# Kernel optimization log

Hardware: AMD Instinct MI355X
Metric: run time of the kernel (lower is better)

## Reference

```python
import jax, jax.numpy as jnp
import numpy as np

B, S, V, D, H, L = 256, 512, 32000, 100, 75, 128

def setup_inputs() -> dict:
    key = jax.random.key(0)
    ks = jax.random.split(key, 10)
    def lin(k, out_f, in_f):
        bound = 1.0 / np.sqrt(in_f)
        kw, kb = jax.random.split(k)
        W = jax.random.uniform(kw, (out_f, in_f), jnp.float32, -bound, bound)
        b = jax.random.uniform(kb, (out_f,), jnp.float32, -bound, bound)
        return W, b
    W1, b1 = lin(ks[0], H, D)   # i2h_fc1
    W2, b2 = lin(ks[1], H, H)   # i2h_fc2
    Wo, bo = lin(ks[2], H, H)   # h2o_fc
    Wfc, bfc = lin(ks[3], L, H) # fc
    emb = jax.random.normal(ks[4], (V, D), jnp.float32)
    X = jax.random.randint(ks[5], (B, S), 0, V)
    return {"X": X, "emb": emb, "W1": W1, "b1": b1, "W2": W2, "b2": b2,
            "Wo": Wo, "bo": bo, "Wfc": Wfc, "bfc": bfc}

def reference(X, emb, W1, b1, W2, b2, Wo, bo, Wfc, bfc):
    x = emb[X]                                   # [B,S,D] embedding lookup (dropout off: is_training=False)
    xp = jnp.einsum('bsd,hd->bsh', x, W1) + b1   # precompute input projection for all steps
    h0 = jnp.zeros((X.shape[0], W2.shape[0]), x.dtype)

    def step(h, xp_t):
        h = jax.nn.sigmoid(xp_t + h @ W2.T + b2)       # Elman hidden update
        o = jax.nn.sigmoid(h @ Wo.T + bo)              # per-step output
        return h, o

    _, outs = jax.lax.scan(step, h0, jnp.swapaxes(xp, 0, 1))  # [S,B,H]
    outs = jnp.swapaxes(outs, 0, 1)                            # [B,S,H] (batch_first)
    return jnp.einsum('bsh,lh->bsl', outs, Wfc) + bfc          # [B,S,L]
```

## Files before the change

### kernel.cpp

```cpp
#include <hip/hip_runtime.h>
#include <hip/hip_bf16.h>

typedef unsigned int uint;
typedef unsigned short ushort;

constexpr int Bn = 256, Sn = 512, Vn = 32000, Dn = 100, Hn = 75, Ln = 128;
constexpr int EW = 80;
constexpr int KP = 96;
constexpr int W2S = 80;

constexpr size_t OFF_EMBW = 0;
constexpr size_t OFF_HALL = OFF_EMBW + (size_t)Vn*EW;
constexpr size_t OFF_W2P  = OFF_HALL + (size_t)Bn*Sn*KP/2;
constexpr size_t OFF_WOH  = OFF_W2P + 3200;
constexpr size_t OFF_WFH  = OFF_WOH + 3840;

typedef __attribute__((ext_vector_type(2))) _Float16 half2_t;
typedef __attribute__((ext_vector_type(8))) _Float16 half8;
typedef __attribute__((ext_vector_type(4))) float floatx4;

__device__ __forceinline__ ushort f2h(float f){
    union { _Float16 h; ushort u; } v; v.h = (_Float16)f; return v.u;
}
__device__ __forceinline__ half8 as_h8(uint4 u){
    union { uint4 u; half8 h; } v; v.u = u; return v.h;
}
__device__ __forceinline__ float sigmoidf(float z){
    return __builtin_amdgcn_rcpf(1.f + __expf(-z));
}

__global__ __launch_bounds__(256) void k_wprep(
    const float* __restrict__ W2, const float* __restrict__ Wo,
    const float* __restrict__ Wfc, ushort* __restrict__ w2p,
    ushort* __restrict__ woh, ushort* __restrict__ wfh, ushort* __restrict__ h_all)
{
    const int tid = blockIdx.x*256 + threadIdx.x;
    const int stride = gridDim.x*256;
    for (int i = tid; i < 80*W2S; i += stride){
        int r = i / W2S, k = i % W2S;
        w2p[i] = (r < Hn && k < Hn) ? f2h(W2[r*Hn + k]) : (ushort)0;
    }
    for (int i = tid; i < 80*KP; i += stride){
        int r = i / KP, k = i % KP;
        woh[i] = (r < Hn && k < Hn) ? f2h(Wo[r*Hn + k]) : (ushort)0;
    }
    for (int i = tid; i < Ln*KP; i += stride){
        int l = i / KP, k = i % KP;
        wfh[i] = (k < Hn) ? f2h(Wfc[l*Hn + k]) : (ushort)0;
    }
    uint* hu = (uint*)h_all;
    for (int i = tid; i < Bn*Sn*8; i += stride){
        int row = i >> 3, c = i & 7;
        hu[(size_t)row*48 + 40 + c] = 0u;
    }
}

__global__ __attribute__((amdgpu_flat_work_group_size(64,64)))
__attribute__((amdgpu_waves_per_eu(1,1)))
void k_embproj(
    const float* __restrict__ emb, const float* __restrict__ W1,
    const float* __restrict__ b1, const float* __restrict__ b2,
    float* __restrict__ embW)
{
    const int lane = threadIdx.x;
    const int v = blockIdx.x*64 + lane;
    const float4* ev = (const float4*)(emb + (size_t)v*Dn);
    float e[Dn];
    #pragma unroll
    for (int q = 0; q < Dn/4; ++q){
        float4 x = ev[q];
        e[4*q] = x.x; e[4*q+1] = x.y; e[4*q+2] = x.z; e[4*q+3] = x.w;
    }
    __shared__ float s_out[64*EW];
    #pragma unroll 4
    for (int j = 0; j < Hn; ++j){
        float a0 = b1[j] + b2[j], a1 = 0.f, a2 = 0.f, a3 = 0.f;
        const float* w = W1 + j*Dn;
        #pragma unroll
        for (int d = 0; d < Dn; d += 4){
            a0 += w[d]*e[d];     a1 += w[d+1]*e[d+1];
            a2 += w[d+2]*e[d+2]; a3 += w[d+3]*e[d+3];
        }
        s_out[lane*EW + j] = (a0+a1) + (a2+a3);
    }
    #pragma unroll
    for (int j = Hn; j < EW; ++j) s_out[lane*EW + j] = 0.f;
    __syncthreads();
    float* dst = embW + (size_t)blockIdx.x*64*EW;
    for (int i = lane; i < 64*EW; i += 64) dst[i] = s_out[i];
}

__global__ __attribute__((amdgpu_flat_work_group_size(64,64)))
__attribute__((amdgpu_waves_per_eu(1,1)))
void k_rnn(
    const int* __restrict__ X, const float* __restrict__ embW,
    const ushort* __restrict__ w2p, ushort* __restrict__ h_all)
{
    const int b = blockIdx.x;
    const int L = threadIdx.x;
    const int m = L & 15;
    const int g = L >> 4;
    __shared__ int sX[Sn];
    __shared__ __align__(16) float xpb[2][64*80];

    for (int i = L; i < Sn; i += 64) sX[i] = X[b*Sn + i];

    half8 bfr[5][3];
    #pragma unroll
    for (int t = 0; t < 5; ++t){
        #pragma unroll
        for (int ks = 0; ks < 3; ++ks){
            int k0 = ks*32 + g*8;
            half8 bv = {};
            if (k0 < 80) bv = *(const half8*)(w2p + (size_t)(16*t + m)*W2S + k0);
            bfr[t][ks] = bv;
        }
    }
    __syncthreads();

    auto stage = [&](int c){
        float* buf = xpb[c & 1];
        const int base = c*64;
        #pragma unroll
        for (int k = 0; k < 20; ++k){
            int idx = k*64 + L;
            int cs  = idx / 20;
            int off = idx - cs*20;
            int tok = sX[base + cs];
            const float* src = embW + (size_t)tok*EW + off*4;
            __builtin_amdgcn_global_load_lds(
                (const __attribute__((address_space(1))) uint*)src,
                (__attribute__((address_space(3))) uint*)(buf + k*256),
                16, 0, 0);
        }
    };

    int va0 = 32*g,      va1 = 32*g + 8,  va2 = 32*g + 16, va3 = 32*g + 24;
    int vb0 = va0 + 128, vb1 = va1 + 128, vb2 = va2 + 128, vb3 = va3 + 128;

    ushort* hout = h_all + (size_t)b*Sn*KP;
    const floatx4 zero4 = {};
    uint4 A0 = {}, A1 = {}, A2 = {};

    stage(0);
    for (int c = 0; c < 8; ++c){
        __syncthreads();
        if (c < 7) stage(c + 1);
        const float* xp = xpb[c & 1];
        float x1c = xp[L];
        float x2c = (L < 16) ? xp[64 + L] : 0.f;
        float x1n = xp[80 + L];
        float x2n = (L < 16) ? xp[80 + 64 + L] : 0.f;
        for (int t = 0; t < 64; ++t){
            int pf = (t + 2 < 64) ? t + 2 : 63;
            float x1f = xp[pf*80 + L];
            float x2f = (L < 16) ? xp[pf*80 + 64 + L] : 0.f;

            half8 af0 = as_h8(A0), af1 = as_h8(A1), af2 = as_h8(A2);

            floatx4 acc0, acc1, acc2, acc3, acc4;
            acc0 = __builtin_amdgcn_mfma_f32_16x16x32_f16(af0, bfr[0][0], zero4, 0,0,0);
            acc1 = __builtin_amdgcn_mfma_f32_16x16x32_f16(af0, bfr[1][0], zero4, 0,0,0);
            acc2 = __builtin_amdgcn_mfma_f32_16x16x32_f16(af0, bfr[2][0], zero4, 0,0,0);
            acc3 = __builtin_amdgcn_mfma_f32_16x16x32_f16(af0, bfr[3][0], zero4, 0,0,0);
            acc4 = __builtin_amdgcn_mfma_f32_16x16x32_f16(af0, bfr[4][0], zero4, 0,0,0);
            acc0 = __builtin_amdgcn_mfma_f32_16x16x32_f16(af1, bfr[0][1], acc0, 0,0,0);
            acc1 = __builtin_amdgcn_mfma_f32_16x16x32_f16(af1, bfr[1][1], acc1, 0,0,0);
            acc2 = __builtin_amdgcn_mfma_f32_16x16x32_f16(af1, bfr[2][1], acc2, 0,0,0);
            acc3 = __builtin_amdgcn_mfma_f32_16x16x32_f16(af1, bfr[3][1], acc3, 0,0,0);
            acc4 = __builtin_amdgcn_mfma_f32_16x16x32_f16(af1, bfr[4][1], acc4, 0,0,0);
            acc0 = __builtin_amdgcn_mfma_f32_16x16x32_f16(af2, bfr[0][2], acc0, 0,0,0);
            acc1 = __builtin_amdgcn_mfma_f32_16x16x32_f16(af2, bfr[1][2], acc1, 0,0,0);
            acc2 = __builtin_amdgcn_mfma_f32_16x16x32_f16(af2, bfr[2][2], acc2, 0,0,0);
            acc3 = __builtin_amdgcn_mfma_f32_16x16x32_f16(af2, bfr[3][2], acc3, 0,0,0);
            acc4 = __builtin_amdgcn_mfma_f32_16x16x32_f16(af2, bfr[4][2], acc4, 0,0,0);

            float y1 = (L < 32) ? ((L < 16) ? acc0[0] : acc1[0])
                                : ((L < 48) ? acc2[0] : acc3[0]);
            float y2 = acc4[0];

            float h1 = sigmoidf(y1 + x1c);
            float h2 = sigmoidf(y2 + x2c);
            if (L >= 11) h2 = 0.f;
            ushort u1 = f2h(h1);
            ushort u2 = f2h(h2);
            int s = c*64 + t;
            hout[(size_t)s*KP + L] = u1;
            if (L < 16) hout[(size_t)s*KP + 64 + L] = u2;

            uint v1 = u1, v2 = u2;
            uint pr1 = (uint)__builtin_amdgcn_update_dpp(0, (int)v1, 0xB1, 0xF, 0xF, true);
            uint pr2 = (uint)__builtin_amdgcn_update_dpp(0, (int)v2, 0xB1, 0xF, 0xF, true);
            int q1 = (int)(v1 | (pr1 << 16));
            int q2 = (int)(v2 | (pr2 << 16));

            A0.x = (uint)__builtin_amdgcn_ds_bpermute(va0, q1);
            A0.y = (uint)__builtin_amdgcn_ds_bpermute(va1, q1);
            A0.z = (uint)__builtin_amdgcn_ds_bpermute(va2, q1);
            A0.w = (uint)__builtin_amdgcn_ds_bpermute(va3, q1);
            A1.x = (uint)__builtin_amdgcn_ds_bpermute(vb0, q1);
            A1.y = (uint)__builtin_amdgcn_ds_bpermute(vb1, q1);
            A1.z = (uint)__builtin_amdgcn_ds_bpermute(vb2, q1);
            A1.w = (uint)__builtin_amdgcn_ds_bpermute(vb3, q1);
            A2.x = (uint)__builtin_amdgcn_ds_bpermute(va0, q2);
            A2.y = (uint)__builtin_amdgcn_ds_bpermute(va1, q2);
            A2.z = (uint)__builtin_amdgcn_ds_bpermute(va2, q2);
            A2.w = (uint)__builtin_amdgcn_ds_bpermute(va3, q2);

            x1c = x1n; x2c = x2n; x1n = x1f; x2n = x2f;
        }
    }
}

__global__ __launch_bounds__(256) void k_out(
    const ushort* __restrict__ h_all, const ushort* __restrict__ woh,
    const ushort* __restrict__ wfh, const float* __restrict__ bo,
    const float* __restrict__ bfc, float* __restrict__ out)
{
    const int lane = threadIdx.x & 63;
    const int w    = threadIdx.x >> 6;
    const size_t r0 = (size_t)blockIdx.x*64 + w*16;
    const int m = lane & 15;
    const int g = lane >> 4;
    __shared__ __align__(16) ushort o_lds[4][16*104];
    ushort* ot = o_lds[w];
    for (int i = lane; i < 128; i += 64){
        int row = i >> 3, cw = i & 7;
        *(uint*)&ot[row*104 + 80 + cw*2] = 0u;
    }
    floatx4 acc1[5] = {};
    const ushort* hbase = h_all + r0*KP;
    #pragma unroll
    for (int ks = 0; ks < 3; ++ks){
        half8 a = *(const half8*)(hbase + (size_t)m*KP + ks*32 + g*8);
        #pragma unroll
        for (int t = 0; t < 5; ++t){
            half8 bt = *(const half8*)(woh + (16*t + m)*KP + ks*32 + g*8);
            acc1[t] = __builtin_amdgcn_mfma_f32_16x16x32_f16(a, bt, acc1[t], 0, 0, 0);
        }
    }
    #pragma unroll
    for (int t = 0; t < 5; ++t){
        int n = 16*t + m;
        float bias = (n < Hn) ? bo[n] : 0.f;
        #pragma unroll
        for (int r = 0; r < 4; ++r){
            int row = g*4 + r;
            float o = 1.f/(1.f + __expf(-(acc1[t][r] + bias)));
            if (n >= Hn) o = 0.f;
            ot[row*104 + n] = f2h(o);
        }
    }
    floatx4 acc2[8] = {};
    #pragma unroll
    for (int ks = 0; ks < 3; ++ks){
        half8 a = *(const half8*)(ot + m*104 + ks*32 + g*8);
        #pragma unroll
        for (int t = 0; t < 8; ++t){
            half8 bt = *(const half8*)(wfh + (16*t + m)*KP + ks*32 + g*8);
            acc2[t] = __builtin_amdgcn_mfma_f32_16x16x32_f16(a, bt, acc2[t], 0, 0, 0);
        }
    }
    float* orow = out + r0*Ln;
    #pragma unroll
    for (int t = 0; t < 8; ++t){
        float bias = bfc[16*t + m];
        #pragma unroll
        for (int r = 0; r < 4; ++r){
            int row = g*4 + r;
            orow[(size_t)row*Ln + 16*t + m] = acc2[t][r] + bias;
        }
    }
}

extern "C" void kernel_launch(void* const* d_in, const int* in_sizes, int n_in,
                              void* d_out, int out_size, void* d_ws, size_t ws_size,
                              hipStream_t stream)
{
    const int*   X   = (const int*)d_in[0];
    const float* emb = (const float*)d_in[1];
    const float* W1  = (const float*)d_in[2];
    const float* b1  = (const float*)d_in[3];
    const float* W2  = (const float*)d_in[4];
    const float* b2  = (const float*)d_in[5];
    const float* Wo  = (const float*)d_in[6];
    const float* bo  = (const float*)d_in[7];
    const float* Wfc = (const float*)d_in[8];
    const float* bfc = (const float*)d_in[9];
    float* out = (float*)d_out;
    float* ws  = (float*)d_ws;

    float*  embW = ws + OFF_EMBW;
    ushort* hall = (ushort*)(ws + OFF_HALL);
    ushort* w2p  = (ushort*)(ws + OFF_W2P);
    ushort* woh  = (ushort*)(ws + OFF_WOH);
    ushort* wfh  = (ushort*)(ws + OFF_WFH);

    k_wprep<<<dim3(512), dim3(256), 0, stream>>>(W2, Wo, Wfc, w2p, woh, wfh, hall);
    k_embproj<<<dim3(Vn/64), dim3(64), 0, stream>>>(emb, W1, b1, b2, embW);
    k_rnn<<<dim3(Bn), dim3(64), 0, stream>>>(X, embW, w2p, hall);
    k_out<<<dim3((Bn*Sn)/64), dim3(256), 0, stream>>>(hall, woh, wfh, bo, bfc, out);
}
```

Measured before the change: 352.8 us.

## Shorten RNN recurrence critical path and split embedding projection across four waves

The recurrent step now computes all five 16-wide hidden chunks in every lane group, with the input projection folded into the MFMA accumulator init. The three K-slices are summed afterwards instead of being chained through the accumulator, which removes the serial MFMA dependency. Hidden-state redistribution now uses v_permlane32_swap plus a single set of bpermute offsets instead of two offset sets. Separately, the embedding projection kernel uses 256 threads, with each wave computing about a quarter of the hidden outputs, to add parallelism per block. The cost is more sigmoid and conversion work per lane, more MFMAs with zero accumulators, and inline asm that depends on gfx950's permlane32 swap.

```diff
diff --git a/kernel.cpp b/kernel.cpp
--- a/kernel.cpp
+++ b/kernel.cpp
@@ -55,14 +55,15 @@
     }
 }
 
-__global__ __attribute__((amdgpu_flat_work_group_size(64,64)))
+__global__ __attribute__((amdgpu_flat_work_group_size(256,256)))
 __attribute__((amdgpu_waves_per_eu(1,1)))
 void k_embproj(
     const float* __restrict__ emb, const float* __restrict__ W1,
     const float* __restrict__ b1, const float* __restrict__ b2,
     float* __restrict__ embW)
 {
-    const int lane = threadIdx.x;
+    const int lane = threadIdx.x & 63;
+    const int w    = threadIdx.x >> 6;
     const int v = blockIdx.x*64 + lane;
     const float4* ev = (const float4*)(emb + (size_t)v*Dn);
     float e[Dn];
@@ -72,22 +73,27 @@
         e[4*q] = x.x; e[4*q+1] = x.y; e[4*q+2] = x.z; e[4*q+3] = x.w;
     }
     __shared__ float s_out[64*EW];
-    #pragma unroll 4
-    for (int j = 0; j < Hn; ++j){
+    const int j0 = w*19;
+    const int jend = (w == 3) ? 18 : 19;
+    #pragma unroll 2
+    for (int jj = 0; jj < jend; ++jj){
+        int j = j0 + jj;
         float a0 = b1[j] + b2[j], a1 = 0.f, a2 = 0.f, a3 = 0.f;
-        const float* w = W1 + j*Dn;
+        const float* wp = W1 + j*Dn;
         #pragma unroll
         for (int d = 0; d < Dn; d += 4){
-            a0 += w[d]*e[d];     a1 += w[d+1]*e[d+1];
-            a2 += w[d+2]*e[d+2]; a3 += w[d+3]*e[d+3];
+            a0 += wp[d]*e[d];     a1 += wp[d+1]*e[d+1];
+            a2 += wp[d+2]*e[d+2]; a3 += wp[d+3]*e[d+3];
         }
         s_out[lane*EW + j] = (a0+a1) + (a2+a3);
     }
-    #pragma unroll
-    for (int j = Hn; j < EW; ++j) s_out[lane*EW + j] = 0.f;
+    if (w == 3){
+        #pragma unroll
+        for (int j = Hn; j < EW; ++j) s_out[lane*EW + j] = 0.f;
+    }
     __syncthreads();
     float* dst = embW + (size_t)blockIdx.x*64*EW;
-    for (int i = lane; i < 64*EW; i += 64) dst[i] = s_out[i];
+    for (int i = threadIdx.x; i < 64*EW; i += 256) dst[i] = s_out[i];
 }
 
 __global__ __attribute__((amdgpu_flat_work_group_size(64,64)))
@@ -135,11 +141,11 @@
         }
     };
 
-    int va0 = 32*g,      va1 = 32*g + 8,  va2 = 32*g + 16, va3 = 32*g + 24;
-    int vb0 = va0 + 128, vb1 = va1 + 128, vb2 = va2 + 128, vb3 = va3 + 128;
+    const int vbase = (L & 32) + ((L & 16) >> 1);
+    const int va0 = 4*(vbase + 0), va1 = 4*(vbase + 2),
+              va2 = 4*(vbase + 4), va3 = 4*(vbase + 6);
 
     ushort* hout = h_all + (size_t)b*Sn*KP;
-    const floatx4 zero4 = {};
     uint4 A0 = {}, A1 = {}, A2 = {};
 
     stage(0);
@@ -147,67 +153,86 @@
         __syncthreads();
         if (c < 7) stage(c + 1);
         const float* xp = xpb[c & 1];
-        float x1c = xp[L];
-        float x2c = (L < 16) ? xp[64 + L] : 0.f;
-        float x1n = xp[80 + L];
-        float x2n = (L < 16) ? xp[80 + 64 + L] : 0.f;
+        float xc0 = xp[m], xc1 = xp[16+m], xc2 = xp[32+m], xc3 = xp[48+m], xc4 = xp[64+m];
+        float xn0 = xp[80+m], xn1 = xp[96+m], xn2 = xp[112+m], xn3 = xp[128+m], xn4 = xp[144+m];
         for (int t = 0; t < 64; ++t){
             int pf = (t + 2 < 64) ? t + 2 : 63;
-            float x1f = xp[pf*80 + L];
-            float x2f = (L < 16) ? xp[pf*80 + 64 + L] : 0.f;
+            const float* xpf = xp + pf*80;
+            float xf0 = xpf[m],    xf1 = xpf[16+m], xf2 = xpf[32+m],
+                  xf3 = xpf[48+m], xf4 = xpf[64+m];
 
             half8 af0 = as_h8(A0), af1 = as_h8(A1), af2 = as_h8(A2);
 
-            floatx4 acc0, acc1, acc2, acc3, acc4;
-            acc0 = __builtin_amdgcn_mfma_f32_16x16x32_f16(af0, bfr[0][0], zero4, 0,0,0);
-            acc1 = __builtin_amdgcn_mfma_f32_16x16x32_f16(af0, bfr[1][0], zero4, 0,0,0);
-            acc2 = __builtin_amdgcn_mfma_f32_16x16x32_f16(af0, bfr[2][0], zero4, 0,0,0);
-            acc3 = __builtin_amdgcn_mfma_f32_16x16x32_f16(af0, bfr[3][0], zero4, 0,0,0);
-            acc4 = __builtin_amdgcn_mfma_f32_16x16x32_f16(af0, bfr[4][0], zero4, 0,0,0);
-            acc0 = __builtin_amdgcn_mfma_f32_16x16x32_f16(af1, bfr[0][1], acc0, 0,0,0);
-            acc1 = __builtin_amdgcn_mfma_f32_16x16x32_f16(af1, bfr[1][1], acc1, 0,0,0);
-            acc2 = __builtin_amdgcn_mfma_f32_16x16x32_f16(af1, bfr[2][1], acc2, 0,0,0);
-            acc3 = __builtin_amdgcn_mfma_f32_16x16x32_f16(af1, bfr[3][1], acc3, 0,0,0);
-            acc4 = __builtin_amdgcn_mfma_f32_16x16x32_f16(af1, bfr[4][1], acc4, 0,0,0);
-            acc0 = __builtin_amdgcn_mfma_f32_16x16x32_f16(af2, bfr[0][2], acc0, 0,0,0);
-            acc1 = __builtin_amdgcn_mfma_f32_16x16x32_f16(af2, bfr[1][2], acc1, 0,0,0);
-            acc2 = __builtin_amdgcn_mfma_f32_16x16x32_f16(af2, bfr[2][2], acc2, 0,0,0);
-            acc3 = __builtin_amdgcn_mfma_f32_16x16x32_f16(af2, bfr[3][2], acc3, 0,0,0);
-            acc4 = __builtin_amdgcn_mfma_f32_16x16x32_f16(af2, bfr[4][2], acc4, 0,0,0);
-
-            float y1 = (L < 32) ? ((L < 16) ? acc0[0] : acc1[0])
-                                : ((L < 48) ? acc2[0] : acc3[0]);
-            float y2 = acc4[0];
-
-            float h1 = sigmoidf(y1 + x1c);
-            float h2 = sigmoidf(y2 + x2c);
-            if (L >= 11) h2 = 0.f;
-            ushort u1 = f2h(h1);
-            ushort u2 = f2h(h2);
+            floatx4 ci0 = {xc0,xc0,xc0,xc0}, ci1 = {xc1,xc1,xc1,xc1},
+                    ci2 = {xc2,xc2,xc2,xc2}, ci3 = {xc3,xc3,xc3,xc3},
+                    ci4 = {xc4,xc4,xc4,xc4};
+            const floatx4 z4 = {};
+            floatx4 p00 = __builtin_amdgcn_mfma_f32_16x16x32_f16(af0, bfr[0][0], ci0, 0,0,0);
+            floatx4 p10 = __builtin_amdgcn_mfma_f32_16x16x32_f16(af0, bfr[1][0], ci1, 0,0,0);
+            floatx4 p20 = __builtin_amdgcn_mfma_f32_16x16x32_f16(af0, bfr[2][0], ci2, 0,0,0);
+            floatx4 p30 = __builtin_amdgcn_mfma_f32_16x16x32_f16(af0, bfr[3][0], ci3, 0,0,0);
+            floatx4 p40 = __builtin_amdgcn_mfma_f32_16x16x32_f16(af0, bfr[4][0], ci4, 0,0,0);
+            floatx4 p01 = __builtin_amdgcn_mfma_f32_16x16x32_f16(af1, bfr[0][1], z4, 0,0,0);
+            floatx4 p11 = __builtin_amdgcn_mfma_f32_16x16x32_f16(af1, bfr[1][1], z4, 0,0,0);
+            floatx4 p21 = __builtin_amdgcn_mfma_f32_16x16x32_f16(af1, bfr[2][1], z4, 0,0,0);
+            floatx4 p31 = __builtin_amdgcn_mfma_f32_16x16x32_f16(af1, bfr[3][1], z4, 0,0,0);
+            floatx4 p41 = __builtin_amdgcn_mfma_f32_16x16x32_f16(af1, bfr[4][1], z4, 0,0,0);
+            floatx4 p02 = __builtin_amdgcn_mfma_f32_16x16x32_f16(af2, bfr[0][2], z4, 0,0,0);
+            floatx4 p12 = __builtin_amdgcn_mfma_f32_16x16x32_f16(af2, bfr[1][2], z4, 0,0,0);
+            floatx4 p22 = __builtin_amdgcn_mfma_f32_16x16x32_f16(af2, bfr[2][2], z4, 0,0,0);
+            floatx4 p32 = __builtin_amdgcn_mfma_f32_16x16x32_f16(af2, bfr[3][2], z4, 0,0,0);
+            floatx4 p42 = __builtin_amdgcn_mfma_f32_16x16x32_f16(af2, bfr[4][2], z4, 0,0,0);
+
+            float h0 = sigmoidf((p00[0] + p01[0]) + p02[0]);
+            float h1 = sigmoidf((p10[0] + p11[0]) + p12[0]);
+            float h2 = sigmoidf((p20[0] + p21[0]) + p22[0]);
+            float h3 = sigmoidf((p30[0] + p31[0]) + p32[0]);
+            float h4 = sigmoidf((p40[0] + p41[0]) + p42[0]);
+            if (m >= 11) h4 = 0.f;
+
+            ushort u0 = f2h(h0), u1 = f2h(h1), u2 = f2h(h2),
+                   u3 = f2h(h3), u4 = f2h(h4);
+
+            ushort us = (L < 32) ? ((L < 16) ? u0 : u1)
+                                 : ((L < 48) ? u2 : u3);
             int s = c*64 + t;
-            hout[(size_t)s*KP + L] = u1;
-            if (L < 16) hout[(size_t)s*KP + 64 + L] = u2;
-
-            uint v1 = u1, v2 = u2;
-            uint pr1 = (uint)__builtin_amdgcn_update_dpp(0, (int)v1, 0xB1, 0xF, 0xF, true);
-            uint pr2 = (uint)__builtin_amdgcn_update_dpp(0, (int)v2, 0xB1, 0xF, 0xF, true);
-            int q1 = (int)(v1 | (pr1 << 16));
-            int q2 = (int)(v2 | (pr2 << 16));
-
-            A0.x = (uint)__builtin_amdgcn_ds_bpermute(va0, q1);
-            A0.y = (uint)__builtin_amdgcn_ds_bpermute(va1, q1);
-            A0.z = (uint)__builtin_amdgcn_ds_bpermute(va2, q1);
-            A0.w = (uint)__builtin_amdgcn_ds_bpermute(va3, q1);
-            A1.x = (uint)__builtin_amdgcn_ds_bpermute(vb0, q1);
-            A1.y = (uint)__builtin_amdgcn_ds_bpermute(vb1, q1);
-            A1.z = (uint)__builtin_amdgcn_ds_bpermute(vb2, q1);
-            A1.w = (uint)__builtin_amdgcn_ds_bpermute(vb3, q1);
-            A2.x = (uint)__builtin_amdgcn_ds_bpermute(va0, q2);
-            A2.y = (uint)__builtin_amdgcn_ds_bpermute(va1, q2);
-            A2.z = (uint)__builtin_amdgcn_ds_bpermute(va2, q2);
-            A2.w = (uint)__builtin_amdgcn_ds_bpermute(va3, q2);
-
-            x1c = x1n; x2c = x2n; x1n = x1f; x2n = x2f;
+            hout[(size_t)s*KP + L] = us;
+            if (L < 16) hout[(size_t)s*KP + 64 + L] = u4;
+
+            uint pq0, pq1, pq2, pq3, pq4;
+            {
+                uint w0=u0, w1=u1, w2=u2, w3=u3, w4=u4;
+                uint r0 = (uint)__builtin_amdgcn_update_dpp(0, (int)w0, 0xB1, 0xF, 0xF, true);
+                uint r1 = (uint)__builtin_amdgcn_update_dpp(0, (int)w1, 0xB1, 0xF, 0xF, true);
+                uint r2 = (uint)__builtin_amdgcn_update_dpp(0, (int)w2, 0xB1, 0xF, 0xF, true);
+                uint r3 = (uint)__builtin_amdgcn_update_dpp(0, (int)w3, 0xB1, 0xF, 0xF, true);
+                uint r4 = (uint)__builtin_amdgcn_update_dpp(0, (int)w4, 0xB1, 0xF, 0xF, true);
+                pq0 = w0 | (r0 << 16); pq1 = w1 | (r1 << 16);
+                pq2 = w2 | (r2 << 16); pq3 = w3 | (r3 << 16);
+                pq4 = w4 | (r4 << 16);
+            }
+            uint S = pq0, Sb = pq1, T = pq2, Tb = pq3, U = pq4, Ub = 0u;
+            asm volatile("s_nop 1\n\t"
+                         "v_permlane32_swap_b32 %0, %1\n\t"
+                         "v_permlane32_swap_b32 %2, %3\n\t"
+                         "v_permlane32_swap_b32 %4, %5"
+                         : "+v"(S), "+v"(Sb), "+v"(T), "+v"(Tb), "+v"(U), "+v"(Ub));
+
+            A0.x = (uint)__builtin_amdgcn_ds_bpermute(va0, (int)S);
+            A0.y = (uint)__builtin_amdgcn_ds_bpermute(va1, (int)S);
+            A0.z = (uint)__builtin_amdgcn_ds_bpermute(va2, (int)S);
+            A0.w = (uint)__builtin_amdgcn_ds_bpermute(va3, (int)S);
+            A1.x = (uint)__builtin_amdgcn_ds_bpermute(va0, (int)T);
+            A1.y = (uint)__builtin_amdgcn_ds_bpermute(va1, (int)T);
+            A1.z = (uint)__builtin_amdgcn_ds_bpermute(va2, (int)T);
+            A1.w = (uint)__builtin_amdgcn_ds_bpermute(va3, (int)T);
+            A2.x = (uint)__builtin_amdgcn_ds_bpermute(va0, (int)U);
+            A2.y = (uint)__builtin_amdgcn_ds_bpermute(va1, (int)U);
+            A2.z = (uint)__builtin_amdgcn_ds_bpermute(va2, (int)U);
+            A2.w = (uint)__builtin_amdgcn_ds_bpermute(va3, (int)U);
+
+            xc0=xn0; xc1=xn1; xc2=xn2; xc3=xn3; xc4=xn4;
+            xn0=xf0; xn1=xf1; xn2=xf2; xn3=xf3; xn4=xf4;
         }
     }
 }
@@ -297,7 +322,7 @@
     ushort* wfh  = (ushort*)(ws + OFF_WFH);
 
     k_wprep<<<dim3(512), dim3(256), 0, stream>>>(W2, Wo, Wfc, w2p, woh, wfh, hall);
-    k_embproj<<<dim3(Vn/64), dim3(64), 0, stream>>>(emb, W1, b1, b2, embW);
+    k_embproj<<<dim3(Vn/64), dim3(256), 0, stream>>>(emb, W1, b1, b2, embW);
     k_rnn<<<dim3(Bn), dim3(64), 0, stream>>>(X, embW, w2p, hall);
     k_out<<<dim3((Bn*Sn)/64), dim3(256), 0, stream>>>(hall, woh, wfh, bo, bfc, out);
 }
```

After: 395.8 us. 1.12x slower.

## Fuse output projection into RNN kernel and widen embedding projection blocks

Applied to the files above, without the earlier changes.

The output-head kernel is folded into the tail of the recurrent kernel. Each block now has four waves: wave 0 runs the sequential recurrence, all four waves share the embedding staging, and after the loop all four compute the output head for their batch row. The embedding projection kernel is also split across four waves by hidden unit. This removes one launch and spreads projection work across more waves. The cost is that three waves sit idle during the recurrence, and the output head, previously spread over many blocks, now runs on only 256 blocks after the serial part ends.

```diff
diff --git a/kernel.cpp b/kernel.cpp
--- a/kernel.cpp
+++ b/kernel.cpp
@@ -55,14 +55,15 @@
     }
 }
 
-__global__ __attribute__((amdgpu_flat_work_group_size(64,64)))
+__global__ __attribute__((amdgpu_flat_work_group_size(256,256)))
 __attribute__((amdgpu_waves_per_eu(1,1)))
 void k_embproj(
     const float* __restrict__ emb, const float* __restrict__ W1,
     const float* __restrict__ b1, const float* __restrict__ b2,
     float* __restrict__ embW)
 {
-    const int lane = threadIdx.x;
+    const int lane = threadIdx.x & 63;
+    const int w    = threadIdx.x >> 6;
     const int v = blockIdx.x*64 + lane;
     const float4* ev = (const float4*)(emb + (size_t)v*Dn);
     float e[Dn];
@@ -72,48 +73,61 @@
         e[4*q] = x.x; e[4*q+1] = x.y; e[4*q+2] = x.z; e[4*q+3] = x.w;
     }
     __shared__ float s_out[64*EW];
-    #pragma unroll 4
-    for (int j = 0; j < Hn; ++j){
+    const int j0 = w*19;
+    const int jend = (w == 3) ? 18 : 19;
+    #pragma unroll 2
+    for (int jj = 0; jj < jend; ++jj){
+        int j = j0 + jj;
         float a0 = b1[j] + b2[j], a1 = 0.f, a2 = 0.f, a3 = 0.f;
-        const float* w = W1 + j*Dn;
+        const float* wp = W1 + j*Dn;
         #pragma unroll
         for (int d = 0; d < Dn; d += 4){
-            a0 += w[d]*e[d];     a1 += w[d+1]*e[d+1];
-            a2 += w[d+2]*e[d+2]; a3 += w[d+3]*e[d+3];
+            a0 += wp[d]*e[d];     a1 += wp[d+1]*e[d+1];
+            a2 += wp[d+2]*e[d+2]; a3 += wp[d+3]*e[d+3];
         }
         s_out[lane*EW + j] = (a0+a1) + (a2+a3);
     }
-    #pragma unroll
-    for (int j = Hn; j < EW; ++j) s_out[lane*EW + j] = 0.f;
+    if (w == 3){
+        #pragma unroll
+        for (int j = Hn; j < EW; ++j) s_out[lane*EW + j] = 0.f;
+    }
     __syncthreads();
     float* dst = embW + (size_t)blockIdx.x*64*EW;
-    for (int i = lane; i < 64*EW; i += 64) dst[i] = s_out[i];
-}
-
-__global__ __attribute__((amdgpu_flat_work_group_size(64,64)))
+    for (int i = threadIdx.x; i < 64*EW; i += 256) dst[i] = s_out[i];
+}
+
+__global__ __attribute__((amdgpu_flat_work_group_size(256,256)))
 __attribute__((amdgpu_waves_per_eu(1,1)))
 void k_rnn(
     const int* __restrict__ X, const float* __restrict__ embW,
-    const ushort* __restrict__ w2p, ushort* __restrict__ h_all)
+    const ushort* __restrict__ w2p, ushort* __restrict__ h_all,
+    const ushort* __restrict__ woh, const ushort* __restrict__ wfh,
+    const float* __restrict__ bo, const float* __restrict__ bfc,
+    float* __restrict__ out)
 {
-    const int b = blockIdx.x;
-    const int L = threadIdx.x;
-    const int m = L & 15;
-    const int g = L >> 4;
+    const int b   = blockIdx.x;
+    const int tid = threadIdx.x;
+    const int L   = tid & 63;
+    const int wv  = tid >> 6;
+    const int m   = L & 15;
+    const int g   = L >> 4;
     __shared__ int sX[Sn];
     __shared__ __align__(16) float xpb[2][64*80];
-
-    for (int i = L; i < Sn; i += 64) sX[i] = X[b*Sn + i];
+    __shared__ __align__(16) ushort o_lds[4][16*104];
+
+    for (int i = tid; i < Sn; i += 256) sX[i] = X[b*Sn + i];
 
     half8 bfr[5][3];
-    #pragma unroll
-    for (int t = 0; t < 5; ++t){
-        #pragma unroll
-        for (int ks = 0; ks < 3; ++ks){
-            int k0 = ks*32 + g*8;
-            half8 bv = {};
-            if (k0 < 80) bv = *(const half8*)(w2p + (size_t)(16*t + m)*W2S + k0);
-            bfr[t][ks] = bv;
+    if (wv == 0){
+        #pragma unroll
+        for (int t = 0; t < 5; ++t){
+            #pragma unroll
+            for (int ks = 0; ks < 3; ++ks){
+                int k0 = ks*32 + g*8;
+                half8 bv = {};
+                if (k0 < 80) bv = *(const half8*)(w2p + (size_t)(16*t + m)*W2S + k0);
+                bfr[t][ks] = bv;
+            }
         }
     }
     __syncthreads();
@@ -122,15 +136,15 @@
         float* buf = xpb[c & 1];
         const int base = c*64;
         #pragma unroll
-        for (int k = 0; k < 20; ++k){
-            int idx = k*64 + L;
+        for (int k = 0; k < 5; ++k){
+            int idx = k*256 + tid;
             int cs  = idx / 20;
             int off = idx - cs*20;
             int tok = sX[base + cs];
             const float* src = embW + (size_t)tok*EW + off*4;
             __builtin_amdgcn_global_load_lds(
                 (const __attribute__((address_space(1))) uint*)src,
-                (__attribute__((address_space(3))) uint*)(buf + k*256),
+                (__attribute__((address_space(3))) uint*)(buf + idx*4),
                 16, 0, 0);
         }
     };
@@ -146,129 +160,123 @@
     for (int c = 0; c < 8; ++c){
         __syncthreads();
         if (c < 7) stage(c + 1);
-        const float* xp = xpb[c & 1];
-        float x1c = xp[L];
-        float x2c = (L < 16) ? xp[64 + L] : 0.f;
-        float x1n = xp[80 + L];
-        float x2n = (L < 16) ? xp[80 + 64 + L] : 0.f;
-        for (int t = 0; t < 64; ++t){
-            int pf = (t + 2 < 64) ? t + 2 : 63;
-            float x1f = xp[pf*80 + L];
-            float x2f = (L < 16) ? xp[pf*80 + 64 + L] : 0.f;
-
-            half8 af0 = as_h8(A0), af1 = as_h8(A1), af2 = as_h8(A2);
-
-            floatx4 acc0, acc1, acc2, acc3, acc4;
-            acc0 = __builtin_amdgcn_mfma_f32_16x16x32_f16(af0, bfr[0][0], zero4, 0,0,0);
-            acc1 = __builtin_amdgcn_mfma_f32_16x16x32_f16(af0, bfr[1][0], zero4, 0,0,0);
-            acc2 = __builtin_amdgcn_mfma_f32_16x16x32_f16(af0, bfr[2][0], zero4, 0,0,0);
-            acc3 = __builtin_amdgcn_mfma_f32_16x16x32_f16(af0, bfr[3][0], zero4, 0,0,0);
-            acc4 = __builtin_amdgcn_mfma_f32_16x16x32_f16(af0, bfr[4][0], zero4, 0,0,0);
-            acc0 = __builtin_amdgcn_mfma_f32_16x16x32_f16(af1, bfr[0][1], acc0, 0,0,0);
-            acc1 = __builtin_amdgcn_mfma_f32_16x16x32_f16(af1, bfr[1][1], acc1, 0,0,0);
-            acc2 = __builtin_amdgcn_mfma_f32_16x16x32_f16(af1, bfr[2][1], acc2, 0,0,0);
-            acc3 = __builtin_amdgcn_mfma_f32_16x16x32_f16(af1, bfr[3][1], acc3, 0,0,0);
-            acc4 = __builtin_amdgcn_mfma_f32_16x16x32_f16(af1, bfr[4][1], acc4, 0,0,0);
-            acc0 = __builtin_amdgcn_mfma_f32_16x16x32_f16(af2, bfr[0][2], acc0, 0,0,0);
-            acc1 = __builtin_amdgcn_mfma_f32_16x16x32_f16(af2, bfr[1][2], acc1, 0,0,0);
-            acc2 = __builtin_amdgcn_mfma_f32_16x16x32_f16(af2, bfr[2][2], acc2, 0,0,0);
-            acc3 = __builtin_amdgcn_mfma_f32_16x16x32_f16(af2, bfr[3][2], acc3, 0,0,0);
-            acc4 = __builtin_amdgcn_mfma_f32_16x16x32_f16(af2, bfr[4][2], acc4, 0,0,0);
-
-            float y1 = (L < 32) ? ((L < 16) ? acc0[0] : acc1[0])
-                                : ((L < 48) ? acc2[0] : acc3[0]);
-            float y2 = acc4[0];
-
-            float h1 = sigmoidf(y1 + x1c);
-            float h2 = sigmoidf(y2 + x2c);
-            if (L >= 11) h2 = 0.f;
-            ushort u1 = f2h(h1);
-            ushort u2 = f2h(h2);
-            int s = c*64 + t;
-            hout[(size_t)s*KP + L] = u1;
-            if (L < 16) hout[(size_t)s*KP + 64 + L] = u2;
-
-            uint v1 = u1, v2 = u2;
-            uint pr1 = (uint)__builtin_amdgcn_update_dpp(0, (int)v1, 0xB1, 0xF, 0xF, true);
-            uint pr2 = (uint)__builtin_amdgcn_update_dpp(0, (int)v2, 0xB1, 0xF, 0xF, true);
-            int q1 = (int)(v1 | (pr1 << 16));
-            int q2 = (int)(v2 | (pr2 << 16));
-
-            A0.x = (uint)__builtin_amdgcn_ds_bpermute(va0, q1);
-            A0.y = (uint)__builtin_amdgcn_ds_bpermute(va1, q1);
-            A0.z = (uint)__builtin_amdgcn_ds_bpermute(va2, q1);
-            A0.w = (uint)__builtin_amdgcn_ds_bpermute(va3, q1);
-            A1.x = (uint)__builtin_amdgcn_ds_bpermute(vb0, q1);
-            A1.y = (uint)__builtin_amdgcn_ds_bpermute(vb1, q1);
-            A1.z = (uint)__builtin_amdgcn_ds_bpermute(vb2, q1);
-            A1.w = (uint)__builtin_amdgcn_ds_bpermute(vb3, q1);
-            A2.x = (uint)__builtin_amdgcn_ds_bpermute(va0, q2);
-            A2.y = (uint)__builtin_amdgcn_ds_bpermute(va1, q2);
-            A2.z = (uint)__builtin_amdgcn_ds_bpermute(va2, q2);
-            A2.w = (uint)__builtin_amdgcn_ds_bpermute(va3, q2);
-
-            x1c = x1n; x2c = x2n; x1n = x1f; x2n = x2f;
-        }
-    }
-}
-
-__global__ __launch_bounds__(256) void k_out(
-    const ushort* __restrict__ h_all, const ushort* __restrict__ woh,
-    const ushort* __restrict__ wfh, const float* __restrict__ bo,
-    const float* __restrict__ bfc, float* __restrict__ out)
-{
-    const int lane = threadIdx.x & 63;
-    const int w    = threadIdx.x >> 6;
-    const size_t r0 = (size_t)blockIdx.x*64 + w*16;
-    const int m = lane & 15;
-    const int g = lane >> 4;
-    __shared__ __align__(16) ushort o_lds[4][16*104];
-    ushort* ot = o_lds[w];
-    for (int i = lane; i < 128; i += 64){
+        if (wv == 0){
+            const float* xp = xpb[c & 1];
+            float x1c = xp[L];
+            float x2c = (L < 16) ? xp[64 + L] : 0.f;
+            float x1n = xp[80 + L];
+            float x2n = (L < 16) ? xp[80 + 64 + L] : 0.f;
+            for (int t = 0; t < 64; ++t){
+                int pf = (t + 2 < 64) ? t + 2 : 63;
+                float x1f = xp[pf*80 + L];
+                float x2f = (L < 16) ? xp[pf*80 + 64 + L] : 0.f;
+
+                half8 af0 = as_h8(A0), af1 = as_h8(A1), af2 = as_h8(A2);
+
+                floatx4 acc0, acc1, acc2, acc3, acc4;
+                acc0 = __builtin_amdgcn_mfma_f32_16x16x32_f16(af0, bfr[0][0], zero4, 0,0,0);
+                acc1 = __builtin_amdgcn_mfma_f32_16x16x32_f16(af0, bfr[1][0], zero4, 0,0,0);
+                acc2 = __builtin_amdgcn_mfma_f32_16x16x32_f16(af0, bfr[2][0], zero4, 0,0,0);
+                acc3 = __builtin_amdgcn_mfma_f32_16x16x32_f16(af0, bfr[3][0], zero4, 0,0,0);
+                acc4 = __builtin_amdgcn_mfma_f32_16x16x32_f16(af0, bfr[4][0], zero4, 0,0,0);
+                acc0 = __builtin_amdgcn_mfma_f32_16x16x32_f16(af1, bfr[0][1], acc0, 0,0,0);
+                acc1 = __builtin_amdgcn_mfma_f32_16x16x32_f16(af1, bfr[1][1], acc1, 0,0,0);
+                acc2 = __builtin_amdgcn_mfma_f32_16x16x32_f16(af1, bfr[2][1], acc2, 0,0,0);
+                acc3 = __builtin_amdgcn_mfma_f32_16x16x32_f16(af1, bfr[3][1], acc3, 0,0,0);
+                acc4 = __builtin_amdgcn_mfma_f32_16x16x32_f16(af1, bfr[4][1], acc4, 0,0,0);
+                acc0 = __builtin_amdgcn_mfma_f32_16x16x32_f16(af2, bfr[0][2], acc0, 0,0,0);
+                acc1 = __builtin_amdgcn_mfma_f32_16x16x32_f16(af2, bfr[1][2], acc1, 0,0,0);
+                acc2 = __builtin_amdgcn_mfma_f32_16x16x32_f16(af2, bfr[2][2], acc2, 0,0,0);
+                acc3 = __builtin_amdgcn_mfma_f32_16x16x32_f16(af2, bfr[3][2], acc3, 0,0,0);
+                acc4 = __builtin_amdgcn_mfma_f32_16x16x32_f16(af2, bfr[4][2], acc4, 0,0,0);
+
+                float y1 = (L < 32) ? ((L < 16) ? acc0[0] : acc1[0])
+                                    : ((L < 48) ? acc2[0] : acc3[0]);
+                float y2 = acc4[0];
+
+                float h1 = sigmoidf(y1 + x1c);
+                float h2 = sigmoidf(y2 + x2c);
+                if (L >= 11) h2 = 0.f;
+                ushort u1 = f2h(h1);
+                ushort u2 = f2h(h2);
+                int s = c*64 + t;
+                hout[(size_t)s*KP + L] = u1;
+                if (L < 16) hout[(size_t)s*KP + 64 + L] = u2;
+
+                uint v1 = u1, v2 = u2;
+                uint pr1 = (uint)__builtin_amdgcn_update_dpp(0, (int)v1, 0xB1, 0xF, 0xF, true);
+                uint pr2 = (uint)__builtin_amdgcn_update_dpp(0, (int)v2, 0xB1, 0xF, 0xF, true);
+                int q1 = (int)(v1 | (pr1 << 16));
+                int q2 = (int)(v2 | (pr2 << 16));
+
+                A0.x = (uint)__builtin_amdgcn_ds_bpermute(va0, q1);
+                A0.y = (uint)__builtin_amdgcn_ds_bpermute(va1, q1);
+                A0.z = (uint)__builtin_amdgcn_ds_bpermute(va2, q1);
+                A0.w = (uint)__builtin_amdgcn_ds_bpermute(va3, q1);
+                A1.x = (uint)__builtin_amdgcn_ds_bpermute(vb0, q1);
+                A1.y = (uint)__builtin_amdgcn_ds_bpermute(vb1, q1);
+                A1.z = (uint)__builtin_amdgcn_ds_bpermute(vb2, q1);
+                A1.w = (uint)__builtin_amdgcn_ds_bpermute(vb3, q1);
+                A2.x = (uint)__builtin_amdgcn_ds_bpermute(va0, q2);
+                A2.y = (uint)__builtin_amdgcn_ds_bpermute(va1, q2);
+                A2.z = (uint)__builtin_amdgcn_ds_bpermute(va2, q2);
+                A2.w = (uint)__builtin_amdgcn_ds_bpermute(va3, q2);
+
+                x1c = x1n; x2c = x2n; x1n = x1f; x2n = x2f;
+            }
+        }
+    }
+    __syncthreads();
+
+    ushort* ot = o_lds[wv];
+    for (int i = L; i < 128; i += 64){
         int row = i >> 3, cw = i & 7;
         *(uint*)&ot[row*104 + 80 + cw*2] = 0u;
     }
-    floatx4 acc1[5] = {};
-    const ushort* hbase = h_all + r0*KP;
-    #pragma unroll
-    for (int ks = 0; ks < 3; ++ks){
-        half8 a = *(const half8*)(hbase + (size_t)m*KP + ks*32 + g*8);
+    for (int it = 0; it < 8; ++it){
+        const size_t r0 = (size_t)b*Sn + it*64 + wv*16;
+        floatx4 acc1[5] = {};
+        const ushort* hbase = h_all + r0*KP;
+        #pragma unroll
+        for (int ks = 0; ks < 3; ++ks){
+            half8 a = *(const half8*)(hbase + (size_t)m*KP + ks*32 + g*8);
+            #pragma unroll
+            for (int t = 0; t < 5; ++t){
+                half8 bt = *(const half8*)(woh + (16*t + m)*KP + ks*32 + g*8);
+                acc1[t] = __builtin_amdgcn_mfma_f32_16x16x32_f16(a, bt, acc1[t], 0, 0, 0);
+            }
+        }
         #pragma unroll
         for (int t = 0; t < 5; ++t){
-            half8 bt = *(const half8*)(woh + (16*t + m)*KP + ks*32 + g*8);
-            acc1[t] = __builtin_amdgcn_mfma_f32_16x16x32_f16(a, bt, acc1[t], 0, 0, 0);
-        }
-    }
-    #pragma unroll
-    for (int t = 0; t < 5; ++t){
-        int n = 16*t + m;
-        float bias = (n < Hn) ? bo[n] : 0.f;
-        #pragma unroll
-        for (int r = 0; r < 4; ++r){
-            int row = g*4 + r;
-            float o = 1.f/(1.f + __expf(-(acc1[t][r] + bias)));
-            if (n >= Hn) o = 0.f;
-            ot[row*104 + n] = f2h(o);
-        }
-    }
-    floatx4 acc2[8] = {};
-    #pragma unroll
-    for (int ks = 0; ks < 3; ++ks){
-        half8 a = *(const half8*)(ot + m*104 + ks*32 + g*8);
+            int n = 16*t + m;
+            float bias = (n < Hn) ? bo[n] : 0.f;
+            #pragma unroll
+            for (int r = 0; r < 4; ++r){
+                int row = g*4 + r;
+                float o = sigmoidf(acc1[t][r] + bias);
+                if (n >= Hn) o = 0.f;
+                ot[row*104 + n] = f2h(o);
+            }
+        }
+        floatx4 acc2[8] = {};
+        #pragma unroll
+        for (int ks = 0; ks < 3; ++ks){
+            half8 a = *(const half8*)(ot + m*104 + ks*32 + g*8);
+            #pragma unroll
+            for (int t = 0; t < 8; ++t){
+                half8 bt = *(const half8*)(wfh + (16*t + m)*KP + ks*32 + g*8);
+                acc2[t] = __builtin_amdgcn_mfma_f32_16x16x32_f16(a, bt, acc2[t], 0, 0, 0);
+            }
+        }
+        float* orow = out + r0*Ln;
         #pragma unroll
         for (int t = 0; t < 8; ++t){
-            half8 bt = *(const half8*)(wfh + (16*t + m)*KP + ks*32 + g*8);
-            acc2[t] = __builtin_amdgcn_mfma_f32_16x16x32_f16(a, bt, acc2[t], 0, 0, 0);
-        }
-    }
-    float* orow = out + r0*Ln;
-    #pragma unroll
-    for (int t = 0; t < 8; ++t){
-        float bias = bfc[16*t + m];
-        #pragma unroll
-        for (int r = 0; r < 4; ++r){
-            int row = g*4 + r;
-            orow[(size_t)row*Ln + 16*t + m] = acc2[t][r] + bias;
+            float bias = bfc[16*t + m];
+            #pragma unroll
+            for (int r = 0; r < 4; ++r){
+                int row = g*4 + r;
+                orow[(size_t)row*Ln + 16*t + m] = acc2[t][r] + bias;
+            }
         }
     }
 }
@@ -297,7 +305,6 @@
     ushort* wfh  = (ushort*)(ws + OFF_WFH);
 
     k_wprep<<<dim3(512), dim3(256), 0, stream>>>(W2, Wo, Wfc, w2p, woh, wfh, hall);
-    k_embproj<<<dim3(Vn/64), dim3(64), 0, stream>>>(emb, W1, b1, b2, embW);
-    k_rnn<<<dim3(Bn), dim3(64), 0, stream>>>(X, embW, w2p, hall);
-    k_out<<<dim3((Bn*Sn)/64), dim3(256), 0, stream>>>(hall, woh, wfh, bo, bfc, out);
-}
+    k_embproj<<<dim3(Vn/64), dim3(256), 0, stream>>>(emb, W1, b1, b2, embW);
+    k_rnn<<<dim3(Bn), dim3(256), 0, stream>>>(X, embW, w2p, hall, woh, wfh, bo, bfc, out);
+}
```

New measurement: 316.6 us. -10.3%, faster.
